# Kernel tuning notes

Measured on AMD Instinct MI355X. Metric: run time of the kernel, lower is better.

## Reference

```python
import jax, jax.numpy as jnp
import numpy as np

ALPHA = 0.2  # LeakyReLU negative slope
NEG_INF = -9e15  # matches torch -9000000000000000.0


def setup_inputs() -> dict:
    key = jax.random.key(0)
    k1, k2, k3, k4, k5, k6 = jax.random.split(key, 6)
    N, F_in, F_out = 4096, 512, 256
    adj = jax.random.randint(k1, (N, N), 0, 2, dtype=jnp.int32)
    h = jax.random.normal(k2, (N, F_in), dtype=jnp.float32)
    # proj: Linear(F_in, F_out)
    W = jax.random.normal(k3, (F_in, F_out), dtype=jnp.float32) * (1.0 / np.sqrt(F_in))
    b = jax.random.normal(k4, (F_out,), dtype=jnp.float32) * 0.01
    # proj_a: Linear(2*F_out, 1) split into the two halves acting on src/dst features
    a1 = jax.random.normal(k5, (F_out,), dtype=jnp.float32) * (1.0 / np.sqrt(2 * F_out))
    a2 = jax.random.normal(k6, (F_out,), dtype=jnp.float32) * (1.0 / np.sqrt(2 * F_out))
    a_b = jnp.zeros((), dtype=jnp.float32)
    return {"adj": adj, "h": h, "W": W, "b": b, "a1": a1, "a2": a2, "a_b": a_b}


def reference(adj, h, W, b, a1, a2, a_b):
    # wh = proj(h): [N, F_out]
    wh = h @ W + b
    # Fused form of the N x N x 2F concat + Linear(2F,1):
    # logits[i, j] = wh[i] . a1 + wh[j] . a2 + a_b
    f_src = wh @ a1  # [N]
    f_dst = wh @ a2  # [N]
    e = jax.nn.leaky_relu(f_src[:, None] + f_dst[None, :] + a_b, negative_slope=ALPHA)
    e = jnp.where(adj > 0, e, NEG_INF)
    att = jax.nn.softmax(e, axis=-1)  # F.softmax legacy dim=1 for 2D
    # dropout: inference mode (no-op) for deterministic reference
    out = att @ wh  # [N, F_out]
    return jax.nn.elu(out)  # concat=True
```

## Files before the change

### kernel.cpp

```cpp
#include <hip/hip_runtime.h>

#define NN   4096
#define FIN  512
#define FOUT 256
#define ALPHA 0.2f

typedef __attribute__((ext_vector_type(8))) short short8;
typedef __attribute__((ext_vector_type(4))) float f32x4;
typedef unsigned short u16;
typedef unsigned int u32;

__device__ __forceinline__ u16 f2bf(float x) {
    union { float f; unsigned u; } v; v.f = x;
    unsigned r = v.u + 0x7FFF + ((v.u >> 16) & 1);
    return (u16)(r >> 16);
}

__global__ __launch_bounds__(256) void k_wt(const float* __restrict__ W,
                                            u16* __restrict__ Wt,
                                            float* __restrict__ fs,
                                            float* __restrict__ fd) {
    __shared__ float s[64 * 65];
    const int t  = threadIdx.x;
    const int g  = (blockIdx.y * gridDim.x + blockIdx.x) * 256 + t;
    if (g < NN) fs[g] = 0.f; else fd[g - NN] = 0.f;
    const int f0 = blockIdx.x * 64;
    const int k0 = blockIdx.y * 64;
    #pragma unroll
    for (int p = 0; p < 4; ++p) {
        int q = t + 256 * p, rr = q >> 4, cc = q & 15;
        float4 w4 = *(const float4*)&W[(size_t)(k0 + rr) * FOUT + f0 + cc * 4];
        s[(cc * 4 + 0) * 65 + rr] = w4.x;
        s[(cc * 4 + 1) * 65 + rr] = w4.y;
        s[(cc * 4 + 2) * 65 + rr] = w4.z;
        s[(cc * 4 + 3) * 65 + rr] = w4.w;
    }
    __syncthreads();
    #pragma unroll
    for (int p = 0; p < 4; ++p) {
        int q = t + 256 * p, f = q >> 4, kg = q & 15;
        ushort4 o;
        o.x = f2bf(s[f * 65 + kg * 4 + 0]);
        o.y = f2bf(s[f * 65 + kg * 4 + 1]);
        o.z = f2bf(s[f * 65 + kg * 4 + 2]);
        o.w = f2bf(s[f * 65 + kg * 4 + 3]);
        *(ushort4*)&Wt[(size_t)(f0 + f) * FIN + k0 + kg * 4] = o;
    }
}

__global__ __launch_bounds__(256) void k_bits(const int* __restrict__ adj,
                                              unsigned long long* __restrict__ bits) {
    const int t = threadIdx.x, l = t & 63;
    const int row = blockIdx.x * 4 + (t >> 6);
    const size_t base = (size_t)row * NN;
    #pragma unroll 4
    for (int o = 0; o < 16; ++o) {
        unsigned long long b0 = __ballot(adj[base + (o * 4 + 0) * 64 + l] > 0);
        unsigned long long b1 = __ballot(adj[base + (o * 4 + 1) * 64 + l] > 0);
        unsigned long long b2 = __ballot(adj[base + (o * 4 + 2) * 64 + l] > 0);
        unsigned long long b3 = __ballot(adj[base + (o * 4 + 3) * 64 + l] > 0);
        if (l == 0) {
            unsigned long long* d = bits + (size_t)row * 64 + o * 4;
            d[0] = b0; d[1] = b1; d[2] = b2; d[3] = b3;
        }
    }
}

#define HS 520
__global__ __launch_bounds__(256) void k_proj(const float* __restrict__ h,
                                              const u16* __restrict__ Wt,
                                              const float* __restrict__ bias,
                                              const float* __restrict__ a1,
                                              const float* __restrict__ a2,
                                              u16* __restrict__ whT,
                                              float* __restrict__ fs,
                                              float* __restrict__ fd) {
    __shared__ u16 s_h[32 * HS];
    const int t  = threadIdx.x;
    const int f0 = blockIdx.x * 64;
    const int i0 = blockIdx.y * 32;
    #pragma unroll
    for (int p = 0; p < 16; ++p) {
        int q = t + 256 * p, row = q >> 7, c4 = q & 127;
        float4 v = *(const float4*)&h[(size_t)(i0 + row) * FIN + c4 * 4];
        ushort4 o; o.x = f2bf(v.x); o.y = f2bf(v.y); o.z = f2bf(v.z); o.w = f2bf(v.w);
        *(ushort4*)&s_h[row * HS + c4 * 4] = o;
    }
    __syncthreads();
    const int w = t >> 6, l = t & 63, n = l & 15, quad = l >> 4;
    const int hh = w & 1, fh = w >> 1;
    f32x4 acc[2] = {{0.f,0.f,0.f,0.f},{0.f,0.f,0.f,0.f}};
    #pragma unroll
    for (int k0 = 0; k0 < FIN; k0 += 32) {
        short8 a = *(const short8*)&s_h[(hh * 16 + n) * HS + k0 + quad * 8];
        short8 b0 = *(const short8*)&Wt[(size_t)(f0 + fh * 32 + n) * FIN + k0 + quad * 8];
        short8 b1 = *(const short8*)&Wt[(size_t)(f0 + fh * 32 + 16 + n) * FIN + k0 + quad * 8];
        acc[0] = __builtin_amdgcn_mfma_f32_16x16x32_bf16(a, b0, acc[0], 0, 0, 0);
        acc[1] = __builtin_amdgcn_mfma_f32_16x16x32_bf16(a, b1, acc[1], 0, 0, 0);
    }
    const int fb = f0 + fh * 32 + n;
    const float bv0 = bias[fb],  bv1 = bias[fb + 16];
    const float a10 = a1[fb],    a11 = a1[fb + 16];
    const float a20 = a2[fb],    a21 = a2[fb + 16];
    u16* wt_tile = whT + (size_t)(i0 >> 5) * (FOUT * 32);
    float d1[4], d2[4];
    #pragma unroll
    for (int r = 0; r < 4; ++r) {
        const int ic = hh * 16 + quad * 4 + r;
        const float v0 = acc[0][r] + bv0;
        const float v1 = acc[1][r] + bv1;
        wt_tile[fb * 32 + ic]        = f2bf(v0);
        wt_tile[(fb + 16) * 32 + ic] = f2bf(v1);
        d1[r] = v0 * a10 + v1 * a11;
        d2[r] = v0 * a20 + v1 * a21;
    }
    #pragma unroll
    for (int m = 1; m < 16; m <<= 1) {
        #pragma unroll
        for (int r = 0; r < 4; ++r) {
            d1[r] += __shfl_xor(d1[r], m);
            d2[r] += __shfl_xor(d2[r], m);
        }
    }
    if (n == 0) {
        #pragma unroll
        for (int r = 0; r < 4; ++r) {
            const int i = i0 + hh * 16 + quad * 4 + r;
            atomicAdd(&fs[i], d1[r]);
            atomicAdd(&fd[i], d2[r]);
        }
    }
}

__global__ __launch_bounds__(256) void k_exp(const float* __restrict__ fd,
                                             float* __restrict__ Fj,
                                             float* __restrict__ Hj) {
    const int g = blockIdx.x * 256 + threadIdx.x;
    float4 v = ((const float4*)fd)[g];
    float4 F, H;
    F.x = __expf(v.x); F.y = __expf(v.y); F.z = __expf(v.z); F.w = __expf(v.w);
    H.x = __expf(ALPHA * v.x); H.y = __expf(ALPHA * v.y);
    H.z = __expf(ALPHA * v.z); H.w = __expf(ALPHA * v.w);
    ((float4*)Fj)[g] = F;
    ((float4*)Hj)[g] = H;
}

#define BI 32
#define CJ 8
__global__ __launch_bounds__(256) void k_attn(const u32* __restrict__ bits,
                                              const u16* __restrict__ whT,
                                              const float* __restrict__ fs,
                                              const float* __restrict__ Fj,
                                              const float* __restrict__ Hj,
                                              const float* __restrict__ ab,
                                              float* __restrict__ part,
                                              float* __restrict__ psum) {
    const int t = threadIdx.x;
    const int w = t >> 6, l = t & 63, n = l & 15, quad = l >> 4;
    const int i0 = blockIdx.x * BI;
    const int c  = blockIdx.y;
    const int jbeg = c * (NN / CJ), jend = jbeg + (NN / CJ);
    const int fw  = w * 64;
    const int jq8 = quad * 8;

    const float abv = ab[0];
    const float s0 = fs[i0 + n] + abv;
    const float s1 = fs[i0 + 16 + n] + abv;
    const float E0 = __expf(s0), G0 = __expf(ALPHA * s0);
    const float E1 = __expf(s1), G1 = __expf(ALPHA * s1);

    f32x4 acc[2][4] = {{{0.f,0.f,0.f,0.f},{0.f,0.f,0.f,0.f},{0.f,0.f,0.f,0.f},{0.f,0.f,0.f,0.f}},
                       {{0.f,0.f,0.f,0.f},{0.f,0.f,0.f,0.f},{0.f,0.f,0.f,0.f},{0.f,0.f,0.f,0.f}}};
    float rs0 = 0.f, rs1 = 0.f;

    const u32* B0 = bits + (size_t)(i0 + n) * 128;
    const u32* B1 = bits + (size_t)(i0 + 16 + n) * 128;
    uint4 m0 = *(const uint4*)&B0[jbeg >> 5];
    uint4 m1 = *(const uint4*)&B1[jbeg >> 5];

#define PEL(FV, HV, BW, K, E, G, OO, IDX, RS) do {            \
        float _p = fmaxf((E) * (FV), (G) * (HV));             \
        _p = ((BW) & (1u << (K))) ? _p : 0.f;                 \
        OO.e[IDX] = f2bf(_p); RS += _p; } while (0)

    for (int jb = jbeg; jb < jend; jb += 128) {
        const uint4 cm0 = m0, cm1 = m1;
        if (jb + 128 < jend) {
            m0 = *(const uint4*)&B0[(jb + 128) >> 5];
            m1 = *(const uint4*)&B1[(jb + 128) >> 5];
        }
        #pragma unroll
        for (int s = 0; s < 4; ++s) {
            const int j0 = jb + s * 32;
            const u32 bw0 = (s == 0 ? cm0.x : s == 1 ? cm0.y : s == 2 ? cm0.z : cm0.w) >> jq8;
            const u32 bw1 = (s == 0 ? cm1.x : s == 1 ? cm1.y : s == 2 ? cm1.z : cm1.w) >> jq8;
            const u16* tb = whT + (size_t)(j0 >> 5) * (FOUT * 32) + quad * 8;
            short8 b[4];
            #pragma unroll
            for (int u = 0; u < 4; ++u)
                b[u] = *(const short8*)&tb[(fw + u * 16 + n) * 32];
            float4 Fa = *(const float4*)&Fj[j0 + jq8];
            float4 Fb = *(const float4*)&Fj[j0 + jq8 + 4];
            float4 Ha = *(const float4*)&Hj[j0 + jq8];
            float4 Hb = *(const float4*)&Hj[j0 + jq8 + 4];
            union { short8 v; u16 e[8]; } o0, o1;
            PEL(Fa.x, Ha.x, bw0, 0, E0, G0, o0, 0, rs0);
            PEL(Fa.y, Ha.y, bw0, 1, E0, G0, o0, 1, rs0);
            PEL(Fa.z, Ha.z, bw0, 2, E0, G0, o0, 2, rs0);
            PEL(Fa.w, Ha.w, bw0, 3, E0, G0, o0, 3, rs0);
            PEL(Fb.x, Hb.x, bw0, 4, E0, G0, o0, 4, rs0);
            PEL(Fb.y, Hb.y, bw0, 5, E0, G0, o0, 5, rs0);
            PEL(Fb.z, Hb.z, bw0, 6, E0, G0, o0, 6, rs0);
            PEL(Fb.w, Hb.w, bw0, 7, E0, G0, o0, 7, rs0);
            PEL(Fa.x, Ha.x, bw1, 0, E1, G1, o1, 0, rs1);
            PEL(Fa.y, Ha.y, bw1, 1, E1, G1, o1, 1, rs1);
            PEL(Fa.z, Ha.z, bw1, 2, E1, G1, o1, 2, rs1);
            PEL(Fa.w, Ha.w, bw1, 3, E1, G1, o1, 3, rs1);
            PEL(Fb.x, Hb.x, bw1, 4, E1, G1, o1, 4, rs1);
            PEL(Fb.y, Hb.y, bw1, 5, E1, G1, o1, 5, rs1);
            PEL(Fb.z, Hb.z, bw1, 6, E1, G1, o1, 6, rs1);
            PEL(Fb.w, Hb.w, bw1, 7, E1, G1, o1, 7, rs1);
            #pragma unroll
            for (int u = 0; u < 4; ++u) {
                acc[0][u] = __builtin_amdgcn_mfma_f32_16x16x32_bf16(o0.v, b[u], acc[0][u], 0, 0, 0);
                acc[1][u] = __builtin_amdgcn_mfma_f32_16x16x32_bf16(o1.v, b[u], acc[1][u], 0, 0, 0);
            }
        }
    }
#undef PEL
    rs0 += __shfl_xor(rs0, 16); rs0 += __shfl_xor(rs0, 32);
    rs1 += __shfl_xor(rs1, 16); rs1 += __shfl_xor(rs1, 32);
    if (w == 0 && quad == 0) {
        psum[(size_t)c * NN + i0 + n]      = rs0;
        psum[(size_t)c * NN + i0 + 16 + n] = rs1;
    }
    float* pc = part + ((size_t)c * NN + i0) * FOUT;
    #pragma unroll
    for (int hf = 0; hf < 2; ++hf)
        #pragma unroll
        for (int u = 0; u < 4; ++u)
            #pragma unroll
            for (int r = 0; r < 4; ++r)
                pc[(size_t)(hf * 16 + quad * 4 + r) * FOUT + fw + u * 16 + n] = acc[hf][u][r];
}

__global__ __launch_bounds__(256) void k_fin(const float* __restrict__ part,
                                             const float* __restrict__ psum,
                                             float* __restrict__ out, int C) {
    const int g = blockIdx.x * 256 + threadIdx.x;
    const int i = g >> 6;
    const size_t s4 = (size_t)NN * FOUT / 4;
    float4 a = ((const float4*)part)[g];
    float s = psum[i];
    for (int c = 1; c < C; ++c) {
        float4 bb = ((const float4*)part)[g + (size_t)c * s4];
        a.x += bb.x; a.y += bb.y; a.z += bb.z; a.w += bb.w;
        s += psum[(size_t)c * NN + i];
    }
    const float inv = 1.0f / s;
    a.x *= inv; a.y *= inv; a.z *= inv; a.w *= inv;
    a.x = a.x > 0.f ? a.x : __expf(a.x) - 1.f;
    a.y = a.y > 0.f ? a.y : __expf(a.y) - 1.f;
    a.z = a.z > 0.f ? a.z : __expf(a.z) - 1.f;
    a.w = a.w > 0.f ? a.w : __expf(a.w) - 1.f;
    ((float4*)out)[g] = a;
}

extern "C" void kernel_launch(void* const* d_in, const int* in_sizes, int n_in,
                              void* d_out, int out_size, void* d_ws, size_t ws_size,
                              hipStream_t stream) {
    const int*   adj = (const int*)  d_in[0];
    const float* h   = (const float*)d_in[1];
    const float* W   = (const float*)d_in[2];
    const float* b   = (const float*)d_in[3];
    const float* a1  = (const float*)d_in[4];
    const float* a2  = (const float*)d_in[5];
    const float* ab  = (const float*)d_in[6];
    float* out = (float*)d_out;

    const int C = CJ;

    float* fs   = (float*)d_ws;
    float* fd   = fs + NN;
    float* Fjv  = fd + NN;
    float* Hjv  = Fjv + NN;
    float* psum = Hjv + NN;
    float* part = psum + (size_t)C * NN;
    u16*   Wt   = (u16*)(part + (size_t)C * NN * FOUT);
    u16*   whT  = Wt + (size_t)FOUT * FIN;
    unsigned long long* bits = (unsigned long long*)(whT + (size_t)NN * FOUT);

    k_wt  <<<dim3(FOUT / 64, FIN / 64), 256, 0, stream>>>(W, Wt, fs, fd);
    k_bits<<<NN / 4, 256, 0, stream>>>(adj, bits);
    k_proj<<<dim3(FOUT / 64, NN / 32), 256, 0, stream>>>(h, Wt, b, a1, a2, whT, fs, fd);
    k_exp <<<NN / 1024, 256, 0, stream>>>(fd, Fjv, Hjv);
    k_attn<<<dim3(NN / BI, C), 256, 0, stream>>>((const u32*)bits, whT, fs, Fjv, Hjv, ab, part, psum);
    k_fin <<<(NN * FOUT / 4) / 256, 256, 0, stream>>>(part, psum, out, C);
}
```

Before: 171.0 us.

## Fuse adjacency bitpacking into projection and exp into attention, double-buffer whT loads

Folds the adjacency-to-bitmask packing into the projection kernel, with each block packing 8 rows. The separate exp kernel goes away because each attention block now computes exp(fd) and exp(alpha*fd) for its column chunk into shared memory. The attention loop is restructured to double-buffer the whT B-fragment loads across 32-column steps, uses packed v_cvt_pk_bf16_f32 conversions, and raises wave priority around the MFMA bursts. This cuts two kernel launches and overlaps global loads with compute. In exchange, the exp work is repeated in every attention block and the projection kernel takes on extra memory-bound work.

```diff
diff --git a/kernel.cpp b/kernel.cpp
--- a/kernel.cpp
+++ b/kernel.cpp
@@ -9,6 +9,7 @@
 typedef __attribute__((ext_vector_type(4))) float f32x4;
 typedef unsigned short u16;
 typedef unsigned int u32;
+typedef unsigned long long u64;
 
 __device__ __forceinline__ u16 f2bf(float x) {
     union { float f; unsigned u; } v; v.f = x;
@@ -48,33 +49,17 @@
     }
 }
 
-__global__ __launch_bounds__(256) void k_bits(const int* __restrict__ adj,
-                                              unsigned long long* __restrict__ bits) {
-    const int t = threadIdx.x, l = t & 63;
-    const int row = blockIdx.x * 4 + (t >> 6);
-    const size_t base = (size_t)row * NN;
-    #pragma unroll 4
-    for (int o = 0; o < 16; ++o) {
-        unsigned long long b0 = __ballot(adj[base + (o * 4 + 0) * 64 + l] > 0);
-        unsigned long long b1 = __ballot(adj[base + (o * 4 + 1) * 64 + l] > 0);
-        unsigned long long b2 = __ballot(adj[base + (o * 4 + 2) * 64 + l] > 0);
-        unsigned long long b3 = __ballot(adj[base + (o * 4 + 3) * 64 + l] > 0);
-        if (l == 0) {
-            unsigned long long* d = bits + (size_t)row * 64 + o * 4;
-            d[0] = b0; d[1] = b1; d[2] = b2; d[3] = b3;
-        }
-    }
-}
-
 #define HS 520
 __global__ __launch_bounds__(256) void k_proj(const float* __restrict__ h,
                                               const u16* __restrict__ Wt,
                                               const float* __restrict__ bias,
                                               const float* __restrict__ a1,
                                               const float* __restrict__ a2,
+                                              const int* __restrict__ adj,
                                               u16* __restrict__ whT,
                                               float* __restrict__ fs,
-                                              float* __restrict__ fd) {
+                                              float* __restrict__ fd,
+                                              u64* __restrict__ bits) {
     __shared__ u16 s_h[32 * HS];
     const int t  = threadIdx.x;
     const int f0 = blockIdx.x * 64;
@@ -130,31 +115,95 @@
             atomicAdd(&fd[i], d2[r]);
         }
     }
-}
-
-__global__ __launch_bounds__(256) void k_exp(const float* __restrict__ fd,
-                                             float* __restrict__ Fj,
-                                             float* __restrict__ Hj) {
-    const int g = blockIdx.x * 256 + threadIdx.x;
-    float4 v = ((const float4*)fd)[g];
-    float4 F, H;
-    F.x = __expf(v.x); F.y = __expf(v.y); F.z = __expf(v.z); F.w = __expf(v.w);
-    H.x = __expf(ALPHA * v.x); H.y = __expf(ALPHA * v.y);
-    H.z = __expf(ALPHA * v.z); H.w = __expf(ALPHA * v.w);
-    ((float4*)Fj)[g] = F;
-    ((float4*)Hj)[g] = H;
+    {
+        const int rr = i0 + (blockIdx.x << 3) + (w << 1);
+        #pragma unroll
+        for (int s = 0; s < 2; ++s) {
+            const size_t ab = (size_t)(rr + s) * NN;
+            u64* dst = bits + (size_t)(rr + s) * 64;
+            #pragma unroll 2
+            for (int o = 0; o < 16; ++o) {
+                u64 q0 = __ballot(adj[ab + (o * 4 + 0) * 64 + l] > 0);
+                u64 q1 = __ballot(adj[ab + (o * 4 + 1) * 64 + l] > 0);
+                u64 q2 = __ballot(adj[ab + (o * 4 + 2) * 64 + l] > 0);
+                u64 q3 = __ballot(adj[ab + (o * 4 + 3) * 64 + l] > 0);
+                if (l == 0) {
+                    dst[o * 4 + 0] = q0;
+                    dst[o * 4 + 1] = q1;
+                    dst[o * 4 + 2] = q2;
+                    dst[o * 4 + 3] = q3;
+                }
+            }
+        }
+    }
 }
 
 #define BI 32
 #define CJ 8
+
+__device__ __forceinline__ void comp_step(
+        const short8& b0, const short8& b1, const short8& b2, const short8& b3,
+        const float* s_F, const float* s_H, int joff, int jq8,
+        u32 w0, u32 w1, float E0, float G0, float E1, float G1,
+        f32x4 (&acc)[2][4], float& rs0, float& rs1) {
+    const float4 Fa = *(const float4*)&s_F[joff + jq8];
+    const float4 Fb = *(const float4*)&s_F[joff + jq8 + 4];
+    const float4 Ha = *(const float4*)&s_H[joff + jq8];
+    const float4 Hb = *(const float4*)&s_H[joff + jq8 + 4];
+    const u32 bw0 = w0 >> jq8, bw1 = w1 >> jq8;
+    float q0, q1, q2, q3, q4, q5, q6, q7;
+    u32 d0, d1, d2, d3;
+    union { short8 v; u32 d[4]; } o0, o1;
+#define PEL1(FV, HV, BW, K, E, G, RS, PP) do { \
+        float _m = fmaxf((E) * (FV), (G) * (HV)); \
+        PP = ((BW) & (1u << (K))) ? _m : 0.f; RS += PP; } while (0)
+    PEL1(Fa.x, Ha.x, bw0, 0, E0, G0, rs0, q0);
+    PEL1(Fa.y, Ha.y, bw0, 1, E0, G0, rs0, q1);
+    PEL1(Fa.z, Ha.z, bw0, 2, E0, G0, rs0, q2);
+    PEL1(Fa.w, Ha.w, bw0, 3, E0, G0, rs0, q3);
+    PEL1(Fb.x, Hb.x, bw0, 4, E0, G0, rs0, q4);
+    PEL1(Fb.y, Hb.y, bw0, 5, E0, G0, rs0, q5);
+    PEL1(Fb.z, Hb.z, bw0, 6, E0, G0, rs0, q6);
+    PEL1(Fb.w, Hb.w, bw0, 7, E0, G0, rs0, q7);
+    asm("v_cvt_pk_bf16_f32 %0, %1, %2" : "=v"(d0) : "v"(q0), "v"(q1));
+    asm("v_cvt_pk_bf16_f32 %0, %1, %2" : "=v"(d1) : "v"(q2), "v"(q3));
+    asm("v_cvt_pk_bf16_f32 %0, %1, %2" : "=v"(d2) : "v"(q4), "v"(q5));
+    asm("v_cvt_pk_bf16_f32 %0, %1, %2" : "=v"(d3) : "v"(q6), "v"(q7));
+    o0.d[0] = d0; o0.d[1] = d1; o0.d[2] = d2; o0.d[3] = d3;
+    PEL1(Fa.x, Ha.x, bw1, 0, E1, G1, rs1, q0);
+    PEL1(Fa.y, Ha.y, bw1, 1, E1, G1, rs1, q1);
+    PEL1(Fa.z, Ha.z, bw1, 2, E1, G1, rs1, q2);
+    PEL1(Fa.w, Ha.w, bw1, 3, E1, G1, rs1, q3);
+    PEL1(Fb.x, Hb.x, bw1, 4, E1, G1, rs1, q4);
+    PEL1(Fb.y, Hb.y, bw1, 5, E1, G1, rs1, q5);
+    PEL1(Fb.z, Hb.z, bw1, 6, E1, G1, rs1, q6);
+    PEL1(Fb.w, Hb.w, bw1, 7, E1, G1, rs1, q7);
+#undef PEL1
+    asm("v_cvt_pk_bf16_f32 %0, %1, %2" : "=v"(d0) : "v"(q0), "v"(q1));
+    asm("v_cvt_pk_bf16_f32 %0, %1, %2" : "=v"(d1) : "v"(q2), "v"(q3));
+    asm("v_cvt_pk_bf16_f32 %0, %1, %2" : "=v"(d2) : "v"(q4), "v"(q5));
+    asm("v_cvt_pk_bf16_f32 %0, %1, %2" : "=v"(d3) : "v"(q6), "v"(q7));
+    o1.d[0] = d0; o1.d[1] = d1; o1.d[2] = d2; o1.d[3] = d3;
+    __builtin_amdgcn_s_setprio(1);
+    acc[0][0] = __builtin_amdgcn_mfma_f32_16x16x32_bf16(o0.v, b0, acc[0][0], 0, 0, 0);
+    acc[0][1] = __builtin_amdgcn_mfma_f32_16x16x32_bf16(o0.v, b1, acc[0][1], 0, 0, 0);
+    acc[0][2] = __builtin_amdgcn_mfma_f32_16x16x32_bf16(o0.v, b2, acc[0][2], 0, 0, 0);
+    acc[0][3] = __builtin_amdgcn_mfma_f32_16x16x32_bf16(o0.v, b3, acc[0][3], 0, 0, 0);
+    acc[1][0] = __builtin_amdgcn_mfma_f32_16x16x32_bf16(o1.v, b0, acc[1][0], 0, 0, 0);
+    acc[1][1] = __builtin_amdgcn_mfma_f32_16x16x32_bf16(o1.v, b1, acc[1][1], 0, 0, 0);
+    acc[1][2] = __builtin_amdgcn_mfma_f32_16x16x32_bf16(o1.v, b2, acc[1][2], 0, 0, 0);
+    acc[1][3] = __builtin_amdgcn_mfma_f32_16x16x32_bf16(o1.v, b3, acc[1][3], 0, 0, 0);
+    __builtin_amdgcn_s_setprio(0);
+}
+
 __global__ __launch_bounds__(256) void k_attn(const u32* __restrict__ bits,
                                               const u16* __restrict__ whT,
                                               const float* __restrict__ fs,
-                                              const float* __restrict__ Fj,
-                                              const float* __restrict__ Hj,
+                                              const float* __restrict__ fd,
                                               const float* __restrict__ ab,
                                               float* __restrict__ part,
                                               float* __restrict__ psum) {
+    __shared__ float s_F[NN / CJ], s_H[NN / CJ];
     const int t = threadIdx.x;
     const int w = t >> 6, l = t & 63, n = l & 15, quad = l >> 4;
     const int i0 = blockIdx.x * BI;
@@ -169,65 +218,52 @@
     const float E0 = __expf(s0), G0 = __expf(ALPHA * s0);
     const float E1 = __expf(s1), G1 = __expf(ALPHA * s1);
 
-    f32x4 acc[2][4] = {{{0.f,0.f,0.f,0.f},{0.f,0.f,0.f,0.f},{0.f,0.f,0.f,0.f},{0.f,0.f,0.f,0.f}},
-                       {{0.f,0.f,0.f,0.f},{0.f,0.f,0.f,0.f},{0.f,0.f,0.f,0.f},{0.f,0.f,0.f,0.f}}};
-    float rs0 = 0.f, rs1 = 0.f;
-
     const u32* B0 = bits + (size_t)(i0 + n) * 128;
     const u32* B1 = bits + (size_t)(i0 + 16 + n) * 128;
     uint4 m0 = *(const uint4*)&B0[jbeg >> 5];
     uint4 m1 = *(const uint4*)&B1[jbeg >> 5];
 
-#define PEL(FV, HV, BW, K, E, G, OO, IDX, RS) do {            \
-        float _p = fmaxf((E) * (FV), (G) * (HV));             \
-        _p = ((BW) & (1u << (K))) ? _p : 0.f;                 \
-        OO.e[IDX] = f2bf(_p); RS += _p; } while (0)
-
+    short8 Ab0, Ab1, Ab2, Ab3, Bb0, Bb1, Bb2, Bb3;
+#define LDB(P, J0) do { const u16* tb_ = whT + (size_t)((J0) >> 5) * (FOUT * 32) + quad * 8; \
+        P##0 = *(const short8*)&tb_[(fw + n) * 32]; \
+        P##1 = *(const short8*)&tb_[(fw + n + 16) * 32]; \
+        P##2 = *(const short8*)&tb_[(fw + n + 32) * 32]; \
+        P##3 = *(const short8*)&tb_[(fw + n + 48) * 32]; } while (0)
+
+    LDB(Ab, jbeg);
+
+    if (t < 128) {
+        float4 v = *(const float4*)&fd[jbeg + t * 4];
+        float4 F, H;
+        F.x = __expf(v.x); F.y = __expf(v.y); F.z = __expf(v.z); F.w = __expf(v.w);
+        H.x = __expf(ALPHA * v.x); H.y = __expf(ALPHA * v.y);
+        H.z = __expf(ALPHA * v.z); H.w = __expf(ALPHA * v.w);
+        *(float4*)&s_F[t * 4] = F;
+        *(float4*)&s_H[t * 4] = H;
+    }
+    __syncthreads();
+
+    f32x4 acc[2][4] = {{{0.f,0.f,0.f,0.f},{0.f,0.f,0.f,0.f},{0.f,0.f,0.f,0.f},{0.f,0.f,0.f,0.f}},
+                       {{0.f,0.f,0.f,0.f},{0.f,0.f,0.f,0.f},{0.f,0.f,0.f,0.f},{0.f,0.f,0.f,0.f}}};
+    float rs0 = 0.f, rs1 = 0.f;
+
+    #pragma unroll 1
     for (int jb = jbeg; jb < jend; jb += 128) {
         const uint4 cm0 = m0, cm1 = m1;
         if (jb + 128 < jend) {
             m0 = *(const uint4*)&B0[(jb + 128) >> 5];
             m1 = *(const uint4*)&B1[(jb + 128) >> 5];
         }
-        #pragma unroll
-        for (int s = 0; s < 4; ++s) {
-            const int j0 = jb + s * 32;
-            const u32 bw0 = (s == 0 ? cm0.x : s == 1 ? cm0.y : s == 2 ? cm0.z : cm0.w) >> jq8;
-            const u32 bw1 = (s == 0 ? cm1.x : s == 1 ? cm1.y : s == 2 ? cm1.z : cm1.w) >> jq8;
-            const u16* tb = whT + (size_t)(j0 >> 5) * (FOUT * 32) + quad * 8;
-            short8 b[4];
-            #pragma unroll
-            for (int u = 0; u < 4; ++u)
-                b[u] = *(const short8*)&tb[(fw + u * 16 + n) * 32];
-            float4 Fa = *(const float4*)&Fj[j0 + jq8];
-            float4 Fb = *(const float4*)&Fj[j0 + jq8 + 4];
-            float4 Ha = *(const float4*)&Hj[j0 + jq8];
-            float4 Hb = *(const float4*)&Hj[j0 + jq8 + 4];
-            union { short8 v; u16 e[8]; } o0, o1;
-            PEL(Fa.x, Ha.x, bw0, 0, E0, G0, o0, 0, rs0);
-            PEL(Fa.y, Ha.y, bw0, 1, E0, G0, o0, 1, rs0);
-            PEL(Fa.z, Ha.z, bw0, 2, E0, G0, o0, 2, rs0);
-            PEL(Fa.w, Ha.w, bw0, 3, E0, G0, o0, 3, rs0);
-            PEL(Fb.x, Hb.x, bw0, 4, E0, G0, o0, 4, rs0);
-            PEL(Fb.y, Hb.y, bw0, 5, E0, G0, o0, 5, rs0);
-            PEL(Fb.z, Hb.z, bw0, 6, E0, G0, o0, 6, rs0);
-            PEL(Fb.w, Hb.w, bw0, 7, E0, G0, o0, 7, rs0);
-            PEL(Fa.x, Ha.x, bw1, 0, E1, G1, o1, 0, rs1);
-            PEL(Fa.y, Ha.y, bw1, 1, E1, G1, o1, 1, rs1);
-            PEL(Fa.z, Ha.z, bw1, 2, E1, G1, o1, 2, rs1);
-            PEL(Fa.w, Ha.w, bw1, 3, E1, G1, o1, 3, rs1);
-            PEL(Fb.x, Hb.x, bw1, 4, E1, G1, o1, 4, rs1);
-            PEL(Fb.y, Hb.y, bw1, 5, E1, G1, o1, 5, rs1);
-            PEL(Fb.z, Hb.z, bw1, 6, E1, G1, o1, 6, rs1);
-            PEL(Fb.w, Hb.w, bw1, 7, E1, G1, o1, 7, rs1);
-            #pragma unroll
-            for (int u = 0; u < 4; ++u) {
-                acc[0][u] = __builtin_amdgcn_mfma_f32_16x16x32_bf16(o0.v, b[u], acc[0][u], 0, 0, 0);
-                acc[1][u] = __builtin_amdgcn_mfma_f32_16x16x32_bf16(o1.v, b[u], acc[1][u], 0, 0, 0);
-            }
-        }
-    }
-#undef PEL
+        LDB(Bb, jb + 32);
+        comp_step(Ab0, Ab1, Ab2, Ab3, s_F, s_H, jb - jbeg,      jq8, cm0.x, cm1.x, E0, G0, E1, G1, acc, rs0, rs1);
+        LDB(Ab, jb + 64);
+        comp_step(Bb0, Bb1, Bb2, Bb3, s_F, s_H, jb - jbeg + 32, jq8, cm0.y, cm1.y, E0, G0, E1, G1, acc, rs0, rs1);
+        LDB(Bb, jb + 96);
+        comp_step(Ab0, Ab1, Ab2, Ab3, s_F, s_H, jb - jbeg + 64, jq8, cm0.z, cm1.z, E0, G0, E1, G1, acc, rs0, rs1);
+        if (jb + 128 < jend) LDB(Ab, jb + 128);
+        comp_step(Bb0, Bb1, Bb2, Bb3, s_F, s_H, jb - jbeg + 96, jq8, cm0.w, cm1.w, E0, G0, E1, G1, acc, rs0, rs1);
+    }
+#undef LDB
     rs0 += __shfl_xor(rs0, 16); rs0 += __shfl_xor(rs0, 32);
     rs1 += __shfl_xor(rs1, 16); rs1 += __shfl_xor(rs1, 32);
     if (w == 0 && quad == 0) {
@@ -282,18 +318,14 @@
 
     float* fs   = (float*)d_ws;
     float* fd   = fs + NN;
-    float* Fjv  = fd + NN;
-    float* Hjv  = Fjv + NN;
-    float* psum = Hjv + NN;
+    float* psum = fd + NN;
     float* part = psum + (size_t)C * NN;
     u16*   Wt   = (u16*)(part + (size_t)C * NN * FOUT);
     u16*   whT  = Wt + (size_t)FOUT * FIN;
-    unsigned long long* bits = (unsigned long long*)(whT + (size_t)NN * FOUT);
+    u64*   bits = (u64*)(whT + (size_t)NN * FOUT);
 
     k_wt  <<<dim3(FOUT / 64, FIN / 64), 256, 0, stream>>>(W, Wt, fs, fd);
-    k_bits<<<NN / 4, 256, 0, stream>>>(adj, bits);
-    k_proj<<<dim3(FOUT / 64, NN / 32), 256, 0, stream>>>(h, Wt, b, a1, a2, whT, fs, fd);
-    k_exp <<<NN / 1024, 256, 0, stream>>>(fd, Fjv, Hjv);
-    k_attn<<<dim3(NN / BI, C), 256, 0, stream>>>((const u32*)bits, whT, fs, Fjv, Hjv, ab, part, psum);
+    k_proj<<<dim3(FOUT / 64, NN / 32), 256, 0, stream>>>(h, Wt, b, a1, a2, adj, whT, fs, fd, bits);
+    k_attn<<<dim3(NN / BI, CJ), 256, 0, stream>>>((const u32*)bits, whT, fs, fd, ab, part, psum);
     k_fin <<<(NN * FOUT / 4) / 256, 256, 0, stream>>>(part, psum, out, C);
 }
```

Measured after the change: 167.8 us. No clear change (-1.9%).
